# Performance work log

Hardware: AMD Instinct MI355X
Metric: run time of the kernel (lower is better)

Reference implementation:

```python
import jax, jax.numpy as jnp
import numpy as np

N = 100_000      # nodes
E = 1_600_000    # edges (before self-loops)
IN_DIM = 128
HID = 64
NEG_SLOPE = 0.2  # PyG GATConv default


def gat_layer(x, src, dst, W, att_src, att_dst, bias, heads, out_ch):
    """PyG-style GATConv: messages flow src -> dst, softmax over incoming edges of dst."""
    n = x.shape[0]
    h = (x @ W).reshape(n, heads, out_ch)                 # [N,H,C]
    a_src = jnp.einsum('nhc,hc->nh', h, att_src)          # [N,H]
    a_dst = jnp.einsum('nhc,hc->nh', h, att_dst)          # [N,H]
    e = jax.nn.leaky_relu(a_src[src] + a_dst[dst], NEG_SLOPE)  # [E,H]
    # segment softmax over edges grouped by destination node
    m = jax.ops.segment_max(e, dst, num_segments=n)       # [N,H]
    ex = jnp.exp(e - m[dst])                              # [E,H]
    denom = jax.ops.segment_sum(ex, dst, num_segments=n)  # [N,H]
    alpha = ex / denom[dst]                               # [E,H]
    msg = alpha[:, :, None] * h[src]                      # [E,H,C]
    out = jax.ops.segment_sum(msg, dst, num_segments=n)   # [N,H,C]
    return out.reshape(n, heads * out_ch) + bias


def setup_inputs() -> dict:
    key = jax.random.key(0)
    ks = jax.random.split(key, 12)
    s = 0.1
    x = jax.random.normal(ks[0], (N, IN_DIM), jnp.float32)
    edge_index = jax.random.randint(ks[1], (2, E), 0, N, dtype=jnp.int32)
    # conv1: in_dim -> hidden, heads=2 (concat)
    W1 = jax.random.normal(ks[2], (IN_DIM, 2 * HID), jnp.float32) * s
    att_src1 = jax.random.normal(ks[3], (2, HID), jnp.float32) * s
    att_dst1 = jax.random.normal(ks[4], (2, HID), jnp.float32) * s
    b1 = jnp.zeros((2 * HID,), jnp.float32)
    # conv2: 2*hidden -> 1, heads=1
    W2 = jax.random.normal(ks[5], (2 * HID, 1), jnp.float32) * s
    att_src2 = jax.random.normal(ks[6], (1, 1), jnp.float32) * s
    att_dst2 = jax.random.normal(ks[7], (1, 1), jnp.float32) * s
    b2 = jnp.zeros((1,), jnp.float32)
    return {"x": x, "edge_index": edge_index,
            "W1": W1, "att_src1": att_src1, "att_dst1": att_dst1, "b1": b1,
            "W2": W2, "att_src2": att_src2, "att_dst2": att_dst2, "b2": b2}


def reference(x, edge_index, W1, att_src1, att_dst1, b1, W2, att_src2, att_dst2, b2):
    n = x.shape[0]
    # PyG GATConv default: add self-loops
    loop = jnp.arange(n, dtype=edge_index.dtype)
    src = jnp.concatenate([edge_index[0], loop])
    dst = jnp.concatenate([edge_index[1], loop])
    h = jax.nn.relu(gat_layer(x, src, dst, W1, att_src1, att_dst1, b1, heads=2, out_ch=HID))
    out = gat_layer(h, src, dst, W2, att_src2, att_dst2, b2, heads=1, out_ch=1)
    return jax.nn.sigmoid(out)  # [N,1]
```

## Files before the change

kernel.cpp:

```cpp
#include <hip/hip_runtime.h>
#include <hip/hip_bf16.h>
#include <hip/hip_fp8.h>
#include <hip/hip_fp16.h>

#define NEG 0.2f
#define CAP 48
#define TILE 2048
typedef unsigned int u32;
typedef unsigned short u16;
typedef unsigned char u8;
typedef unsigned long long u64;
typedef __attribute__((ext_vector_type(8))) short s8v;
typedef __attribute__((ext_vector_type(4))) float f4v;
typedef __attribute__((ext_vector_type(2))) float f2v;

__global__ __launch_bounds__(256) void binA_k(const int* __restrict__ ei,
                                              int2* __restrict__ meta,
                                              u64* __restrict__ slabs,
                                              int E, int Etot, int NB, int ntiles){
  __shared__ int bcnt[512], sc[512], bcur[512];
  int tile = blockIdx.x, tid = threadIdx.x;
  int base = tile*TILE;
  int cnt = min(TILE, Etot - base);
  for (int i=tid;i<512;i+=256) bcnt[i]=0;
  __syncthreads();
  int dd[8], ss[8];
  #pragma unroll
  for (int j=0;j<8;j++){
    int i = tid + j*256;
    if (i < cnt){
      int e = base+i;
      int d = (e<E)? ei[E+e] : e-E;
      int s = (e<E)? ei[e]   : d;
      dd[j] = d; ss[j] = s;
      atomicAdd(&bcnt[d>>8], 1);
    } else dd[j] = -1;
  }
  __syncthreads();
  sc[tid]     = bcnt[tid];
  sc[tid+256] = bcnt[tid+256];
  __syncthreads();
  for (int o=1;o<512;o<<=1){
    int i0=tid, i1=tid+256;
    int r0 = (i0>=o)? sc[i0-o]:0;
    int r1 = (i1>=o)? sc[i1-o]:0;
    __syncthreads();
    sc[i0]+=r0; sc[i1]+=r1;
    __syncthreads();
  }
  bcur[tid]     = sc[tid]     - bcnt[tid];
  bcur[tid+256] = sc[tid+256] - bcnt[tid+256];
  __syncthreads();
  for (int b=tid;b<NB;b+=256)
    meta[(size_t)b*ntiles + tile] = make_int2(sc[b]-bcnt[b], bcnt[b]);
  #pragma unroll
  for (int j=0;j<8;j++){
    if (dd[j] >= 0){
      int p = atomicAdd(&bcur[dd[j]>>8], 1);
      slabs[(size_t)base + p] = ((u64)(u32)dd[j] << 32) | (u32)ss[j];
    }
  }
}

__global__ __launch_bounds__(1024) void binB_k(const u64* __restrict__ slabs,
                                               const int2* __restrict__ meta,
                                               const float2* __restrict__ as1,
                                               const float2* __restrict__ ad1,
                                               int* __restrict__ cur,
                                               u64* __restrict__ combo,
                                               float2* __restrict__ den,
                                               int N, int ntiles){
  int b = blockIdx.x, tid = threadIdx.x;
  int lo = b<<8;
  int nn = min(256, N-lo);
  __shared__ int lcur[256];
  __shared__ float sden0[256], sden1[256];
  __shared__ float2 sad[256];
  if (tid < 256){
    lcur[tid]=0; sden0[tid]=0.f; sden1[tid]=0.f;
    sad[tid] = (tid<nn)? ad1[lo+tid] : make_float2(0.f,0.f);
  }
  __syncthreads();
  int grp = tid>>3, l8 = tid&7;
  const int2* mrow = meta + (size_t)b*ntiles;
  int2 m = (grp < ntiles)? mrow[grp] : make_int2(0,0);
  for (int t=grp; t<ntiles; t+=128){
    int2 mn = (t+128 < ntiles)? mrow[t+128] : make_int2(0,0);
    const u64* sp = slabs + (size_t)t*TILE + m.x;
    for (int i=l8; i<m.y; i+=8){
      u64 pk = sp[i];
      int d = (int)(pk>>32), s = (int)(u32)pk;
      int dl = d & 255;
      float2 av = as1[s];
      float2 adv = sad[dl];
      float e0 = av.x+adv.x; e0 = (e0>0.f)? e0 : NEG*e0;
      float e1 = av.y+adv.y; e1 = (e1>0.f)? e1 : NEG*e1;
      __half2 hw = __floats2half2_rn(__expf(e0), __expf(e1));
      float2 wr = __half22float2(hw);
      atomicAdd(&sden0[dl], wr.x);
      atomicAdd(&sden1[dl], wr.y);
      int p = atomicAdd(&lcur[dl], 1);
      u32 wb = *(u32*)&hw;
      if (p < CAP) combo[(size_t)p*N + d] = ((u64)wb << 32) | (u32)s;
    }
    m = mn;
  }
  __syncthreads();
  if (tid < nn){
    cur[lo+tid] = lcur[tid];
    den[lo+tid] = make_float2(sden0[tid], sden1[tid]);
  }
}

__global__ __launch_bounds__(256) void wt_k(const float* __restrict__ W, u16* __restrict__ Wt){
  int g = blockIdx.x*256 + threadIdx.x;
  int k = g >> 7, c = g & 127;
  __hip_bfloat16 b = __float2bfloat16(W[g]);
  Wt[c*128 + k] = *(u16*)&b;
}

__global__ __launch_bounds__(256) void gemm_k(const float* __restrict__ x,
                                              const u16* __restrict__ Wt,
                                              const float* __restrict__ aw_s,
                                              const float* __restrict__ aw_d,
                                              u8*  __restrict__ h1f,
                                              float2* __restrict__ as1,
                                              float2* __restrict__ ad1, int N){
  __shared__ u16 xs[128*136];
  __shared__ u16 ws[128*136];
  int tid = threadIdx.x;
  int rowBase = blockIdx.x * 128;
  #pragma unroll
  for (int i=0;i<16;i++){
    int j = i*256 + tid;
    int c = j >> 5, k4 = j & 31;
    *(uint2*)&ws[c*136 + k4*4] = ((const uint2*)Wt)[j];
  }
  #pragma unroll
  for (int i=0;i<16;i++){
    int j = i*256 + tid;
    int r = j >> 5, c4 = j & 31;
    float4 v = make_float4(0.f,0.f,0.f,0.f);
    if (rowBase + r < N) v = ((const float4*)x)[(size_t)(rowBase+r)*32 + c4];
    __hip_bfloat16 b0=__float2bfloat16(v.x), b1=__float2bfloat16(v.y);
    __hip_bfloat16 b2=__float2bfloat16(v.z), b3=__float2bfloat16(v.w);
    u32 w0 = (u32)*(u16*)&b0 | ((u32)*(u16*)&b1 << 16);
    u32 w1 = (u32)*(u16*)&b2 | ((u32)*(u16*)&b3 << 16);
    *(uint2*)&xs[r*136 + c4*4] = make_uint2(w0, w1);
  }
  __syncthreads();
  int wv = tid >> 6, lane = tid & 63;
  int lr = lane & 15, lk = lane >> 4;
  f4v acc[2][8];
  #pragma unroll
  for (int rt=0;rt<2;rt++)
    #pragma unroll
    for (int ct=0;ct<8;ct++) acc[rt][ct] = (f4v){0.f,0.f,0.f,0.f};
  #pragma unroll
  for (int ks=0; ks<4; ks++){
    int koff = ks*32 + lk*8;
    s8v bfrag[8];
    #pragma unroll
    for (int ct=0; ct<8; ct++)
      bfrag[ct] = *(s8v*)&ws[(ct*16 + lr)*136 + koff];
    #pragma unroll
    for (int rt=0; rt<2; rt++){
      int row = wv*32 + rt*16 + lr;
      s8v afrag = *(s8v*)&xs[row*136 + koff];
      #pragma unroll
      for (int ct=0; ct<8; ct++)
        acc[rt][ct] = __builtin_amdgcn_mfma_f32_16x16x32_bf16(afrag, bfrag[ct], acc[rt][ct], 0,0,0);
    }
  }
  #pragma unroll
  for (int rt=0; rt<2; rt++){
    float lps0[4]={0,0,0,0}, lps1[4]={0,0,0,0}, lpd0[4]={0,0,0,0}, lpd1[4]={0,0,0,0};
    int nodeB = rowBase + wv*32 + rt*16 + lk*4;
    #pragma unroll
    for (int ct=0; ct<8; ct++){
      int ch = ct*16 + lr;
      float aws = aw_s[ch], awd = aw_d[ch];
      #pragma unroll
      for (int reg=0; reg<4; reg++){
        float v = acc[rt][ct][reg];
        if (ct < 4){ lps0[reg] = fmaf(v, aws, lps0[reg]); lpd0[reg] = fmaf(v, awd, lpd0[reg]); }
        else       { lps1[reg] = fmaf(v, aws, lps1[reg]); lpd1[reg] = fmaf(v, awd, lpd1[reg]); }
      }
      int pk01 = __builtin_amdgcn_cvt_pk_fp8_f32(acc[rt][ct][0], acc[rt][ct][1], 0, false);
      int pk23 = __builtin_amdgcn_cvt_pk_fp8_f32(acc[rt][ct][2], acc[rt][ct][3], 0, false);
      if (nodeB + 0 < N) h1f[(size_t)(nodeB+0)*128 + ch] = (u8)(pk01 & 0xff);
      if (nodeB + 1 < N) h1f[(size_t)(nodeB+1)*128 + ch] = (u8)((pk01 >> 8) & 0xff);
      if (nodeB + 2 < N) h1f[(size_t)(nodeB+2)*128 + ch] = (u8)(pk23 & 0xff);
      if (nodeB + 3 < N) h1f[(size_t)(nodeB+3)*128 + ch] = (u8)((pk23 >> 8) & 0xff);
    }
    #pragma unroll
    for (int reg=0; reg<4; reg++){
      float a=lps0[reg], b=lps1[reg], c=lpd0[reg], d=lpd1[reg];
      #pragma unroll
      for (int o=1;o<16;o<<=1){
        a += __shfl_xor(a,o); b += __shfl_xor(b,o);
        c += __shfl_xor(c,o); d += __shfl_xor(d,o);
      }
      int node = nodeB + reg;
      if (lr == 0 && node < N){
        as1[node] = make_float2(a, b);
        ad1[node] = make_float2(c, d);
      }
    }
  }
}

__global__ __launch_bounds__(256) void agg1_k(const uint2* __restrict__ h1f2,
                                              const u64* __restrict__ combo,
                                              const float2* __restrict__ den,
                                              const int* __restrict__ cur,
                                              const float4* __restrict__ b1_4,
                                              const float4* __restrict__ W2_4,
                                              float* __restrict__ h2, int N){
  int w = threadIdx.x >> 6, l = threadIdx.x & 63;
  int g = l >> 4, li = l & 15;
  int n = blockIdx.x*16 + w*4 + g;
  if (n >= N) return;
  int deg = min(cur[n], CAP);
  bool hsel = (li >= 8);
  float2 dn = den[n];
  float rd = 1.f / (hsel ? dn.y : dn.x);
  float ac0=0.f,ac1=0.f,ac2=0.f,ac3=0.f,ac4=0.f,ac5=0.f,ac6=0.f,ac7=0.f;
  for (int kk = 0; kk < deg; kk += 8){
    u64 pk[8]; bool vd[8];
    #pragma unroll
    for (int j=0;j<8;j++){
      int idx = kk + j;
      vd[j] = idx < deg;
      pk[j] = combo[(size_t)(vd[j] ? idx : 0)*N + n];
    }
    uint2 hv[8];
    #pragma unroll
    for (int j=0;j<8;j++) hv[j] = h1f2[(size_t)(u32)(pk[j] & 0xffffffffu)*16 + li];
    #pragma unroll
    for (int j=0;j<8;j++){
      u32 wb = (u32)(pk[j] >> 32);
      __half2 hw = *(__half2*)&wb;
      float2 wf = __half22float2(hw);
      float gw = hsel ? wf.y : wf.x;
      gw = vd[j] ? gw : 0.f;
      f2v p0 = __builtin_amdgcn_cvt_pk_f32_fp8((int)hv[j].x, false);
      f2v p1 = __builtin_amdgcn_cvt_pk_f32_fp8((int)hv[j].x, true);
      f2v p2 = __builtin_amdgcn_cvt_pk_f32_fp8((int)hv[j].y, false);
      f2v p3 = __builtin_amdgcn_cvt_pk_f32_fp8((int)hv[j].y, true);
      ac0 = fmaf(gw, p0.x, ac0); ac1 = fmaf(gw, p0.y, ac1);
      ac2 = fmaf(gw, p1.x, ac2); ac3 = fmaf(gw, p1.y, ac3);
      ac4 = fmaf(gw, p2.x, ac4); ac5 = fmaf(gw, p2.y, ac5);
      ac6 = fmaf(gw, p3.x, ac6); ac7 = fmaf(gw, p3.y, ac7);
    }
  }
  float4 bb0 = b1_4[li*2], bb1 = b1_4[li*2+1];
  float4 ww0 = W2_4[li*2], ww1 = W2_4[li*2+1];
  float p = 0.f;
  p = fmaf(fmaxf(fmaf(ac0, rd, bb0.x), 0.f), ww0.x, p);
  p = fmaf(fmaxf(fmaf(ac1, rd, bb0.y), 0.f), ww0.y, p);
  p = fmaf(fmaxf(fmaf(ac2, rd, bb0.z), 0.f), ww0.z, p);
  p = fmaf(fmaxf(fmaf(ac3, rd, bb0.w), 0.f), ww0.w, p);
  p = fmaf(fmaxf(fmaf(ac4, rd, bb1.x), 0.f), ww1.x, p);
  p = fmaf(fmaxf(fmaf(ac5, rd, bb1.y), 0.f), ww1.y, p);
  p = fmaf(fmaxf(fmaf(ac6, rd, bb1.z), 0.f), ww1.z, p);
  p = fmaf(fmaxf(fmaf(ac7, rd, bb1.w), 0.f), ww1.w, p);
  #pragma unroll
  for (int o=1;o<16;o<<=1) p += __shfl_xor(p,o);
  if (li == 0) h2[n] = p;
}

__global__ __launch_bounds__(256) void agg2_k(const float* __restrict__ h2,
                                              const int* __restrict__ cur,
                                              const u64* __restrict__ combo,
                                              const float* __restrict__ att_s2,
                                              const float* __restrict__ att_d2,
                                              const float* __restrict__ b2,
                                              float* __restrict__ out, int N){
  int w = threadIdx.x >> 6, l = threadIdx.x & 63;
  int n = blockIdx.x*4 + w;
  if (n >= N) return;
  float as2 = att_s2[0], ad2 = att_d2[0];
  float hd = h2[n]*ad2;
  int deg = min(cur[n], CAP);
  bool v = l < deg;
  int s = (int)(u32)(combo[(size_t)(v ? l : 0)*N + n] & 0xffffffffu);
  float hs = h2[s];
  float e = fmaf(hs, as2, hd); e = (e>0.f)? e : NEG*e;
  float xv = v ? __expf(e) : 0.f;
  float den = xv, wsum = xv*hs;
  #pragma unroll
  for (int o=32;o>0;o>>=1){ den += __shfl_xor(den,o); wsum += __shfl_xor(wsum,o); }
  if (l == 0){
    float z = wsum/den + b2[0];
    out[n] = 1.f/(1.f + __expf(-z));
  }
}

extern "C" void kernel_launch(void* const* d_in, const int* in_sizes, int n_in,
                              void* d_out, int out_size, void* d_ws, size_t ws_size,
                              hipStream_t stream){
  const float* x     = (const float*)d_in[0];
  const int*   ei    = (const int*)d_in[1];
  const float* W1    = (const float*)d_in[2];
  const float* aw_s  = (const float*)d_in[3];
  const float* aw_d  = (const float*)d_in[4];
  const float* b1    = (const float*)d_in[5];
  const float* W2    = (const float*)d_in[6];
  const float* at_s2 = (const float*)d_in[7];
  const float* at_d2 = (const float*)d_in[8];
  const float* b2    = (const float*)d_in[9];
  float* out = (float*)d_out;

  const int N = in_sizes[0]/128;
  const int E = in_sizes[1]/2;
  const int Etot = E + N;
  const int ntiles = (Etot + TILE - 1) / TILE;
  const int NB = (N + 255) >> 8;

  auto align256 = [](size_t v){ return (v + 255) & ~(size_t)255; };
  char* w = (char*)d_ws;
  u8* h1f       = (u8*)w;     w += align256((size_t)N*128);
  float2* as1   = (float2*)w; w += align256((size_t)N*8);
  float2* ad1   = (float2*)w; w += align256((size_t)N*8);
  float* h2     = (float*)w;  w += align256((size_t)N*4);
  int* cur      = (int*)w;    w += align256((size_t)N*4);
  float2* den   = (float2*)w; w += align256((size_t)N*8);
  u16* Wt       = (u16*)w;    w += align256((size_t)128*128*2);
  u64* combo    = (u64*)w;    w += align256((size_t)N*CAP*8);
  u64* slabs    = (u64*)w;    w += align256((size_t)ntiles*TILE*8);
  int2* meta    = (int2*)w;   w += align256((size_t)NB*ntiles*8);

  const int tb = 256;
  binA_k<<<ntiles, tb, 0, stream>>>(ei, meta, slabs, E, Etot, NB, ntiles);
  wt_k<<<64, tb, 0, stream>>>(W1, Wt);
  gemm_k<<<(N+127)/128, tb, 0, stream>>>(x, Wt, aw_s, aw_d, h1f, as1, ad1, N);
  binB_k<<<NB, 1024, 0, stream>>>(slabs, meta, as1, ad1, cur, combo, den, N, ntiles);
  agg1_k<<<(N+15)/16, tb, 0, stream>>>((const uint2*)h1f, combo, den, cur,
                                       (const float4*)b1, (const float4*)W2, h2, N);
  agg2_k<<<(N+3)/4, tb, 0, stream>>>(h2, cur, combo, at_s2, at_d2, b2, out, N);
}
```

Baseline: 156.8 us.

## Store per-node edge lists contiguously via in-block count and prefix scan

binB now makes a counting pass over the binned edge slabs, runs a shared-memory prefix scan to get per-node offsets, and then writes each node's edges contiguously into a block-local region. Before, edges went into a strided [slot][N] layout. A new woff array records each node's start so agg1 and agg2 can read neighbour lists contiguously. The aim is better coalescing in agg2, where lanes walk one node's edges, and more local scatter writes in binB. The cost is a second read of the slabs and extra block-wide syncs for the scan.

```diff
diff --git a/kernel.cpp b/kernel.cpp
--- a/kernel.cpp
+++ b/kernel.cpp
@@ -67,25 +67,46 @@
                                                const float2* __restrict__ as1,
                                                const float2* __restrict__ ad1,
                                                int* __restrict__ cur,
+                                               u32* __restrict__ woff,
                                                u64* __restrict__ combo,
                                                float2* __restrict__ den,
                                                int N, int ntiles){
   int b = blockIdx.x, tid = threadIdx.x;
   int lo = b<<8;
   int nn = min(256, N-lo);
-  __shared__ int lcur[256];
+  __shared__ int lcnt[256], loff[256], lcur[256];
   __shared__ float sden0[256], sden1[256];
   __shared__ float2 sad[256];
   if (tid < 256){
-    lcur[tid]=0; sden0[tid]=0.f; sden1[tid]=0.f;
+    lcnt[tid]=0; sden0[tid]=0.f; sden1[tid]=0.f;
     sad[tid] = (tid<nn)? ad1[lo+tid] : make_float2(0.f,0.f);
   }
   __syncthreads();
   int grp = tid>>3, l8 = tid&7;
   const int2* mrow = meta + (size_t)b*ntiles;
-  int2 m = (grp < ntiles)? mrow[grp] : make_int2(0,0);
   for (int t=grp; t<ntiles; t+=128){
-    int2 mn = (t+128 < ntiles)? mrow[t+128] : make_int2(0,0);
+    int2 m = mrow[t];
+    const u64* sp = slabs + (size_t)t*TILE + m.x;
+    for (int i=l8; i<m.y; i+=8){
+      int d = (int)(sp[i]>>32);
+      atomicAdd(&lcnt[d & 255], 1);
+    }
+  }
+  __syncthreads();
+  if (tid < 256) loff[tid] = lcnt[tid];
+  __syncthreads();
+  for (int o=1;o<256;o<<=1){
+    int v = 0;
+    if (tid < 256 && tid >= o) v = loff[tid-o];
+    __syncthreads();
+    if (tid < 256) loff[tid] += v;
+    __syncthreads();
+  }
+  if (tid < 256) lcur[tid] = loff[tid] - lcnt[tid];
+  __syncthreads();
+  u32 wbase = (u32)b * (256u*CAP);
+  for (int t=grp; t<ntiles; t+=128){
+    int2 m = mrow[t];
     const u64* sp = slabs + (size_t)t*TILE + m.x;
     for (int i=l8; i<m.y; i+=8){
       u64 pk = sp[i];
@@ -100,15 +121,15 @@
       atomicAdd(&sden0[dl], wr.x);
       atomicAdd(&sden1[dl], wr.y);
       int p = atomicAdd(&lcur[dl], 1);
-      u32 wb = *(u32*)&hw;
-      if (p < CAP) combo[(size_t)p*N + d] = ((u64)wb << 32) | (u32)s;
-    }
-    m = mn;
+      u32 wb32 = *(u32*)&hw;
+      combo[(size_t)(wbase + (u32)p)] = ((u64)wb32 << 32) | (u32)s;
+    }
   }
   __syncthreads();
   if (tid < nn){
-    cur[lo+tid] = lcur[tid];
-    den[lo+tid] = make_float2(sden0[tid], sden1[tid]);
+    cur[lo+tid]  = lcnt[tid];
+    woff[lo+tid] = wbase + (u32)(loff[tid] - lcnt[tid]);
+    den[lo+tid]  = make_float2(sden0[tid], sden1[tid]);
   }
 }
 
@@ -212,6 +233,7 @@
 
 __global__ __launch_bounds__(256) void agg1_k(const uint2* __restrict__ h1f2,
                                               const u64* __restrict__ combo,
+                                              const u32* __restrict__ woff,
                                               const float2* __restrict__ den,
                                               const int* __restrict__ cur,
                                               const float4* __restrict__ b1_4,
@@ -222,6 +244,7 @@
   int n = blockIdx.x*16 + w*4 + g;
   if (n >= N) return;
   int deg = min(cur[n], CAP);
+  u32 base = woff[n];
   bool hsel = (li >= 8);
   float2 dn = den[n];
   float rd = 1.f / (hsel ? dn.y : dn.x);
@@ -232,11 +255,14 @@
     for (int j=0;j<8;j++){
       int idx = kk + j;
       vd[j] = idx < deg;
-      pk[j] = combo[(size_t)(vd[j] ? idx : 0)*N + n];
+      pk[j] = combo[(size_t)(base + (u32)(vd[j] ? idx : 0))];
     }
     uint2 hv[8];
     #pragma unroll
-    for (int j=0;j<8;j++) hv[j] = h1f2[(size_t)(u32)(pk[j] & 0xffffffffu)*16 + li];
+    for (int j=0;j<8;j++){
+      u32 off = ((u32)(pk[j] & 0xffffffffu) << 4) | (u32)li;
+      hv[j] = h1f2[off];
+    }
     #pragma unroll
     for (int j=0;j<8;j++){
       u32 wb = (u32)(pk[j] >> 32);
@@ -272,6 +298,7 @@
 
 __global__ __launch_bounds__(256) void agg2_k(const float* __restrict__ h2,
                                               const int* __restrict__ cur,
+                                              const u32* __restrict__ woff,
                                               const u64* __restrict__ combo,
                                               const float* __restrict__ att_s2,
                                               const float* __restrict__ att_d2,
@@ -283,8 +310,9 @@
   float as2 = att_s2[0], ad2 = att_d2[0];
   float hd = h2[n]*ad2;
   int deg = min(cur[n], CAP);
+  u32 base = woff[n];
   bool v = l < deg;
-  int s = (int)(u32)(combo[(size_t)(v ? l : 0)*N + n] & 0xffffffffu);
+  int s = (int)(u32)(combo[(size_t)(base + (u32)(v ? l : 0))] & 0xffffffffu);
   float hs = h2[s];
   float e = fmaf(hs, as2, hd); e = (e>0.f)? e : NEG*e;
   float xv = v ? __expf(e) : 0.f;
@@ -325,9 +353,10 @@
   float2* ad1   = (float2*)w; w += align256((size_t)N*8);
   float* h2     = (float*)w;  w += align256((size_t)N*4);
   int* cur      = (int*)w;    w += align256((size_t)N*4);
+  u32* woff     = (u32*)w;    w += align256((size_t)N*4);
   float2* den   = (float2*)w; w += align256((size_t)N*8);
   u16* Wt       = (u16*)w;    w += align256((size_t)128*128*2);
-  u64* combo    = (u64*)w;    w += align256((size_t)N*CAP*8);
+  u64* combo    = (u64*)w;    w += align256((size_t)NB*256*CAP*8);
   u64* slabs    = (u64*)w;    w += align256((size_t)ntiles*TILE*8);
   int2* meta    = (int2*)w;   w += align256((size_t)NB*ntiles*8);
 
@@ -335,8 +364,8 @@
   binA_k<<<ntiles, tb, 0, stream>>>(ei, meta, slabs, E, Etot, NB, ntiles);
   wt_k<<<64, tb, 0, stream>>>(W1, Wt);
   gemm_k<<<(N+127)/128, tb, 0, stream>>>(x, Wt, aw_s, aw_d, h1f, as1, ad1, N);
-  binB_k<<<NB, 1024, 0, stream>>>(slabs, meta, as1, ad1, cur, combo, den, N, ntiles);
-  agg1_k<<<(N+15)/16, tb, 0, stream>>>((const uint2*)h1f, combo, den, cur,
+  binB_k<<<NB, 1024, 0, stream>>>(slabs, meta, as1, ad1, cur, woff, combo, den, N, ntiles);
+  agg1_k<<<(N+15)/16, tb, 0, stream>>>((const uint2*)h1f, combo, woff, den, cur,
                                        (const float4*)b1, (const float4*)W2, h2, N);
-  agg2_k<<<(N+3)/4, tb, 0, stream>>>(h2, cur, combo, at_s2, at_d2, b2, out, N);
-}
+  agg2_k<<<(N+3)/4, tb, 0, stream>>>(h2, cur, woff, combo, at_s2, at_d2, b2, out, N);
+}
```

Result: slower. 169.7 us (+8.2%).
